# Optimization experiments

Measured on AMD Instinct MI355X. Metric: run time of the kernel, lower is better.

## Reference

```python
import jax, jax.numpy as jnp
import numpy as np

B, N, CS, CZ, CH, H, PQ, PV = 1, 768, 384, 128, 16, 12, 4, 8
INF, EPS, LN_EPS = 1e5, 1e-8, 1e-5


def setup_inputs() -> dict:
    key = jax.random.key(0)
    ks = jax.random.split(key, 16)
    def nrm(k, shape, scale=0.02):
        return jax.random.normal(k, shape, dtype=jnp.float32) * scale
    return {
        "s": jax.random.normal(ks[0], (B, N, CS), jnp.float32),
        "z": jax.random.normal(ks[1], (B, N, N, CZ), jnp.float32),
        "r_rot": jax.random.normal(ks[2], (B, N, 5, 3, 3), jnp.float32),
        "r_trans": jax.random.normal(ks[3], (B, N, 5, 3), jnp.float32),
        "mask": jnp.ones((B, N, 5), jnp.float32),
        "wq": nrm(ks[4], (H * CH, CS)), "bq": jnp.zeros((H * CH,), jnp.float32),
        "wkv": nrm(ks[5], (2 * H * CH, CS)), "bkv": jnp.zeros((2 * H * CH,), jnp.float32),
        "wqp": nrm(ks[6], (H * PQ * 3, CS)), "bqp": jnp.zeros((H * PQ * 3,), jnp.float32),
        "wkvp": nrm(ks[7], (H * (PQ + PV) * 3, CS)), "bkvp": jnp.zeros((H * (PQ + PV) * 3,), jnp.float32),
        "wb": nrm(ks[8], (H, CZ)), "bb": jnp.zeros((H,), jnp.float32),
        "head_w": nrm(ks[9], (H,), 0.5),
        "wout": nrm(ks[10], (CS, H * (CZ + CH + PV * 4))), "bout": jnp.zeros((CS,), jnp.float32),
        "wexp": nrm(ks[11], (5 * CS, CS)), "bexp": jnp.zeros((5 * CS,), jnp.float32),
        "ln_g": jnp.ones((CS,), jnp.float32), "ln_b": jnp.zeros((CS,), jnp.float32),
        "ww": nrm(ks[12], (1, CS)), "bw": jnp.zeros((1,), jnp.float32),
    }


def _mix(x, fg_mask, weight, ndims):
    # x: [B,N,5,...]; weighted blend of backbone frame (index 0) and mean of
    # masked functional-group frames (indices 1:5).
    bb_f = x[:, :, :1]
    m = fg_mask.reshape(fg_mask.shape + (1,) * ndims)
    fg = (x[:, :, 1:] * m).sum(axis=2, keepdims=True)
    denom = fg_mask.sum(-1, keepdims=True).reshape(fg_mask.shape[:2] + (1,) * (ndims + 1))
    fg = fg / (denom + 1e-8)
    w = weight.reshape(weight.shape[:2] + (1,) * (ndims + 1))
    return (w * bb_f + (1.0 - w) * fg)[:, :, 0]


def _ipa(s, z, r_rot, r_trans, mask, wq, bq, wkv, bkv, wqp, bqp, wkvp, bkvp,
         wb, bb, head_w, wout, bout, wexp, bexp, ln_g, ln_b, ww, bw):
    fg_mask = mask[..., 1:]            # [B,N,4]
    ulr = mask[..., 0]                 # [B,N]
    # softmax over a size-1 axis (as in original code -> all ones)
    weight = jax.nn.softmax(s @ ww.T + bw, axis=-1)   # [B,N,1]

    se = (s @ wexp.T + bexp).reshape(B, N, 5, CS)
    mu = se.mean(-1, keepdims=True)
    var = ((se - mu) ** 2).mean(-1, keepdims=True)
    se = (se - mu) * jax.lax.rsqrt(var + LN_EPS) * ln_g + ln_b

    q = _mix((se @ wq.T + bq).reshape(B, N, 5, H, CH), fg_mask, weight, 2)      # [B,N,H,CH]
    kv = _mix((se @ wkv.T + bkv).reshape(B, N, 5, H, 2 * CH), fg_mask, weight, 2)
    k, v = kv[..., :CH], kv[..., CH:]

    def pts_of(w_, b_, npts):
        lin = se @ w_.T + b_                                   # [B,N,5,3*H*npts]
        pts = jnp.moveaxis(lin.reshape(B, N, 5, 3, H * npts), -2, -1)  # [B,N,5,H*npts,3]
        pts = jnp.einsum('bnfij,bnfpj->bnfpi', r_rot, pts) + r_trans[:, :, :, None, :]
        return _mix(pts.reshape(B, N, 5, H, npts, 3), fg_mask, weight, 3)

    q_pts = pts_of(wqp, bqp, PQ)                               # [B,N,H,PQ,3]
    kv_pts = pts_of(wkvp, bkvp, PQ + PV)
    k_pts, v_pts = kv_pts[..., :PQ, :], kv_pts[..., PQ:, :]

    bias = z @ wb.T + bb                                       # [B,N,N,H]
    a = jnp.einsum('bihc,bjhc->bhij', q, k) * (1.0 / (3 * CH)) ** 0.5
    a = a + (1.0 / 3.0) ** 0.5 * jnp.transpose(bias, (0, 3, 1, 2))

    d2 = jnp.sum((q_pts[:, :, None] - k_pts[:, None]) ** 2, axis=-1)  # [B,N,N,H,PQ]
    hw = jax.nn.softplus(head_w) * (1.0 / (3 * (PQ * 9.0 / 2))) ** 0.5
    pt_att = -0.5 * jnp.sum(d2 * hw[:, None], axis=-1)         # [B,N,N,H]
    a = a + jnp.transpose(pt_att, (0, 3, 1, 2))
    sq_mask = INF * (ulr[:, :, None] * ulr[:, None, :] - 1.0)
    a = jax.nn.softmax(a + sq_mask[:, None], axis=-1)          # [B,H,N,N]

    o = jnp.einsum('bhij,bjhc->bihc', a, v).reshape(B, N, H * CH)
    o_pt = jnp.einsum('bhij,bjhpx->bihpx', a, v_pts)           # [B,N,H,PV,3]
    rot0, t0 = r_rot[:, :, 0], r_trans[:, :, 0]                # backbone frame
    # invert_apply: R^T (x - t)
    o_pt = jnp.einsum('bnik,bnhpi->bnhpk', rot0, o_pt - t0[:, :, None, None, :])
    o_pt_norm = jnp.sqrt(jnp.sum(o_pt ** 2, -1) + EPS).reshape(B, N, H * PV)
    o_pt = o_pt.reshape(B, N, H * PV, 3)
    o_pair = jnp.einsum('bhij,bijc->bihc', a, z).reshape(B, N, H * CZ)
    cat = jnp.concatenate([o, o_pt[..., 0], o_pt[..., 1], o_pt[..., 2], o_pt_norm, o_pair], -1)
    return cat @ wout.T + bout                                 # [B,N,CS]


def reference(s, z, r_rot, r_trans, mask, wq, bq, wkv, bkv, wqp, bqp, wkvp, bkvp,
              wb, bb, head_w, wout, bout, wexp, bexp, ln_g, ln_b, ww, bw):
    return _ipa(s, z, r_rot, r_trans, mask, wq, bq, wkv, bkv, wqp, bqp, wkvp, bkvp,
                wb, bb, head_w, wout, bout, wexp, bexp, ln_g, ln_b, ww, bw)
```

## Files before the change

### kernel.cpp

```cpp
#include <hip/hip_runtime.h>
#include <hip/hip_bf16.h>
#include <stdint.h>


typedef float  f32x4 __attribute__((ext_vector_type(4)));
typedef short  s16x8 __attribute__((ext_vector_type(8)));

__device__ __forceinline__ float bf2f(unsigned short u) {
    union { unsigned int i; float f; } v; v.i = ((unsigned int)u) << 16; return v.f;
}
__device__ __forceinline__ unsigned short f2bf(float f) {
    union { float f; unsigned int i; } v; v.f = f;
    unsigned int r = v.i + 0x7fffu + ((v.i >> 16) & 1u);
    return (unsigned short)(r >> 16);
}
__device__ __forceinline__ unsigned packbf2(float a, float b) {
    return (unsigned)f2bf(a) | ((unsigned)f2bf(b) << 16);
}
__device__ __forceinline__ float bval(int c,
    const float* bq, const float* bkv, const float* bqp, const float* bkvp)
{
    if (c < 192)      return bq[c];
    else if (c < 576) return bkv[c - 192];
    else if (c < 720) return bqp[c - 576];
    else              return bkvp[c - 720];
}

__global__ __launch_bounds__(256) void k_prep(
    const float* __restrict__ s, const float* __restrict__ wexp,
    const float* __restrict__ wq, const float* __restrict__ wkv,
    const float* __restrict__ wqp, const float* __restrict__ wkvp,
    const float* __restrict__ wout,
    const float* __restrict__ bq, const float* __restrict__ bkv,
    const float* __restrict__ bqp, const float* __restrict__ bkvp,
    unsigned short* __restrict__ s_bf, unsigned short* __restrict__ we_bf,
    unsigned short* __restrict__ wc_bf, unsigned short* __restrict__ wo_bf,
    float* __restrict__ bcat)
{
    const int x = blockIdx.x * 256 + threadIdx.x;
    if (x >= 1696896) return;
    if (x < 294912)            s_bf[x] = f2bf(s[x]);
    else if (x < 442368)       we_bf[x - 294912] = f2bf(wexp[x - 294912]);
    else if (x < 516096)       wc_bf[x - 442368] = f2bf(wq[x - 442368]);
    else if (x < 663552)       wc_bf[73728 + (x - 516096)] = f2bf(wkv[x - 516096]);
    else if (x < 718848)       wc_bf[221184 + (x - 663552)] = f2bf(wqp[x - 663552]);
    else if (x < 884736)       wc_bf[276480 + (x - 718848)] = f2bf(wkvp[x - 718848]);
    else if (x < 1695744)      wo_bf[x - 884736] = f2bf(wout[x - 884736]);
    else {
        int j = x - 1695744;
        bcat[j] = bval(j, bq, bkv, bqp, bkvp);
    }
}

__global__ __launch_bounds__(256) void k_mm(
    const unsigned short* __restrict__ A, int lda,
    const unsigned short* __restrict__ B, int ldb,
    float* __restrict__ C, int ldc, const float* __restrict__ bias,
    int nk, size_t pstride)
{
    const int m0 = blockIdx.x * 64, n0 = blockIdx.y * 64;
    const int koff = blockIdx.z * nk * 32;
    C += (size_t)blockIdx.z * pstride;
    const int t = threadIdx.x;
    const int lane = t & 63, wave = t >> 6, quad = lane >> 4, lcol = lane & 15;
    const int mh = (wave & 1) * 32, nh = (wave >> 1) * 32;
    __shared__ unsigned short As[64 * 40];
    __shared__ unsigned short Bs[64 * 40];
    const int lr = t >> 2, ls = (t & 3) * 8;
    const unsigned short* Ap = A + (size_t)(m0 + lr) * lda + koff + ls;
    const unsigned short* Bp = B + (size_t)(n0 + lr) * ldb + koff + ls;
    f32x4 acc[2][2] = {};

    uint4 av = *(const uint4*)Ap;
    uint4 bv = *(const uint4*)Bp;
    for (int kc = 0; kc < nk; ++kc) {
        __syncthreads();
        *(uint4*)&As[lr * 40 + ls] = av;
        *(uint4*)&Bs[lr * 40 + ls] = bv;
        __syncthreads();
        if (kc + 1 < nk) {
            av = *(const uint4*)(Ap + (size_t)(kc + 1) * 32);
            bv = *(const uint4*)(Bp + (size_t)(kc + 1) * 32);
        }
        s16x8 af0 = *(const s16x8*)&As[(mh + lcol) * 40 + quad * 8];
        s16x8 af1 = *(const s16x8*)&As[(mh + 16 + lcol) * 40 + quad * 8];
        s16x8 bf0 = *(const s16x8*)&Bs[(nh + lcol) * 40 + quad * 8];
        s16x8 bf1 = *(const s16x8*)&Bs[(nh + 16 + lcol) * 40 + quad * 8];
        acc[0][0] = __builtin_amdgcn_mfma_f32_16x16x32_bf16(af0, bf0, acc[0][0], 0, 0, 0);
        acc[0][1] = __builtin_amdgcn_mfma_f32_16x16x32_bf16(af0, bf1, acc[0][1], 0, 0, 0);
        acc[1][0] = __builtin_amdgcn_mfma_f32_16x16x32_bf16(af1, bf0, acc[1][0], 0, 0, 0);
        acc[1][1] = __builtin_amdgcn_mfma_f32_16x16x32_bf16(af1, bf1, acc[1][1], 0, 0, 0);
    }
    #pragma unroll
    for (int r = 0; r < 2; ++r)
        #pragma unroll
        for (int c = 0; c < 2; ++c) {
            int gn = n0 + nh + c * 16 + lcol;
            float bv2 = bias ? bias[gn] : 0.f;
            #pragma unroll
            for (int ii = 0; ii < 4; ++ii) {
                int gm = m0 + mh + r * 16 + quad * 4 + ii;
                C[(size_t)gm * ldc + gn] = acc[r][c][ii] + bv2;
            }
        }
}

__global__ __launch_bounds__(256) void k_ln(
    const float* __restrict__ se_raw, const float* __restrict__ ln_g,
    const float* __restrict__ ln_b, unsigned short* __restrict__ se0_bf)
{
    const int n = blockIdx.x * 4 + (threadIdx.x >> 6);
    const int lane = threadIdx.x & 63;
    const float* row = se_raw + (size_t)n * 384;
    float v[6], s1 = 0.f, s2 = 0.f;
    #pragma unroll
    for (int q = 0; q < 6; ++q) {
        v[q] = row[lane + q * 64];
        s1 += v[q]; s2 += v[q] * v[q];
    }
    for (int mk = 1; mk < 64; mk <<= 1) {
        s1 += __shfl_xor(s1, mk, 64);
        s2 += __shfl_xor(s2, mk, 64);
    }
    float mu = s1 * (1.f / 384.f);
    float var = s2 * (1.f / 384.f) - mu * mu;
    float rs = rsqrtf(fmaxf(var, 0.f) + 1e-5f);
    unsigned short* orow = se0_bf + (size_t)n * 384;
    #pragma unroll
    for (int q = 0; q < 6; ++q) {
        int c = lane + q * 64;
        orow[c] = f2bf((v[q] - mu) * rs * ln_g[c] + ln_b[c]);
    }
}

__global__ __launch_bounds__(256) void k_post(
    const float* __restrict__ lin,
    const float* __restrict__ r_rot, const float* __restrict__ r_trans,
    float* __restrict__ q_out, unsigned short* __restrict__ k_out,
    float* __restrict__ v_out, float* __restrict__ qp_out,
    unsigned short* __restrict__ kp_out, float* __restrict__ vp_out,
    float* __restrict__ k2_out)
{
    const int n0 = blockIdx.x * 8;
    const int t = threadIdx.x;
    __shared__ float kprot[8 * 144];

    for (int r = 0; r < 8; ++r) {
        const int n = n0 + r;
        const float* lrow = lin + (size_t)n * 1152;
        const float* rot = r_rot + (size_t)n * 45;
        for (int u = t; u < 1152; u += 256) {
            if (u < 192) {
                q_out[(size_t)n * 192 + u] = lrow[u];
            } else if (u < 576) {
                int l2 = u - 192, h = l2 >> 5, c = l2 & 31;
                float v = lrow[u];
                if (c < 16) k_out[(size_t)n * 192 + h * 16 + c] = f2bf(v);
                else        v_out[(size_t)n * 192 + h * 16 + (c - 16)] = v;
            } else {
                int y = u - 576;
                int pt = y / 3, i = y - pt * 3;
                float t0 = r_trans[(size_t)n * 15 + i];
                float v;
                if (pt < 48) {
                    v = rot[i*3+0] * lrow[576 + pt]
                      + rot[i*3+1] * lrow[576 + 48 + pt]
                      + rot[i*3+2] * lrow[576 + 96 + pt] + t0;
                    qp_out[(size_t)n * 144 + pt * 3 + i] = v;
                } else {
                    int pp = pt - 48;
                    v = rot[i*3+0] * lrow[720 + pp]
                      + rot[i*3+1] * lrow[720 + 144 + pp]
                      + rot[i*3+2] * lrow[720 + 288 + pp] + t0;
                    int h = pp / 12, pl = pp - h * 12;
                    if (pl < 4) {
                        kp_out[(size_t)n * 144 + (h * 4 + pl) * 3 + i] = f2bf(v);
                        kprot[r * 144 + (h * 4 + pl) * 3 + i] = v;
                    } else {
                        vp_out[(size_t)n * 288 + (h * 8 + (pl - 4)) * 3 + i] = v;
                    }
                }
            }
        }
    }
    __syncthreads();
    if (t < 96) {
        int r = t / 12, h = t - r * 12;
        float ss = 0.f;
        #pragma unroll
        for (int d = 0; d < 12; ++d) {
            float v = kprot[r * 144 + h * 12 + d];
            ss += v * v;
        }
        k2_out[(size_t)(n0 + r) * 12 + h] = ss;
    }
}

__global__ __launch_bounds__(256) void k_attn(
    const float* __restrict__ z, const float* __restrict__ mask,
    const float* __restrict__ head_w, const float* __restrict__ wb,
    const float* __restrict__ bb,
    const float* __restrict__ q_ws, const float* __restrict__ qp_ws,
    const float* __restrict__ k2_ws,
    const unsigned short* __restrict__ k_bf, const float* __restrict__ v_f,
    const unsigned short* __restrict__ kp_bf, const float* __restrict__ vp_f,
    float* __restrict__ parts)
{
    const int i = blockIdx.x >> 1;
    const int half = blockIdx.x & 1;
    const int t = threadIdx.x;
    const int lane = t & 63, wv = t >> 6;
    const int quad = lane >> 4, lcol = lane & 15;

    __shared__ short zb[64 * 136];
    __shared__ float L[64 * 17];
    __shared__ float Pt[16 * 68];
    __shared__ float qs[192], qps[144];
    __shared__ float ulra[384];
    __shared__ float m_s[16], l_s[16], alph_s[16];

    const float c_qk = 0.14433756729740643f;
    const float c_b  = 0.57735026918962576f;

    if (t < 192) qs[t]  = q_ws[(size_t)i * 192 + t];
    if (t < 144) qps[t] = qp_ws[(size_t)i * 144 + t];
    if (t >= 192 && t < 208) { int u = t - 192; m_s[u] = -1e30f; l_s[u] = 0.f; alph_s[u] = 1.f; }
    for (int x = t; x < 384; x += 256) ulra[x] = mask[(size_t)(half * 384 + x) * 5];
    for (int x = t; x < 4 * 68; x += 256) Pt[12 * 68 + x] = 0.f;
    const float ulr_i = mask[(size_t)i * 5];

    s16x8 wbf[4];
    #pragma unroll
    for (int kb = 0; kb < 4; ++kb) {
        #pragma unroll
        for (int j = 0; j < 8; ++j) {
            int c = kb * 32 + quad * 8 + j;
            wbf[kb][j] = (lcol < 12) ? (short)f2bf(wb[(size_t)lcol * 128 + c]) : (short)0;
        }
    }
    __syncthreads();

    const int hh = (lcol < 12) ? lcol : 11;
    f32x4 qv[4], qpv[3];
    float q2_r = 0.f;
    #pragma unroll
    for (int m = 0; m < 4; ++m) qv[m] = *(const f32x4*)&qs[hh * 16 + m * 4];
    #pragma unroll
    for (int m = 0; m < 3; ++m) {
        qpv[m] = *(const f32x4*)&qps[hh * 12 + m * 4];
        #pragma unroll
        for (int e = 0; e < 4; ++e) q2_r += qpv[m][e] * qpv[m][e];
    }
    float xh = head_w[hh];
    const float cpt_r = -0.5f * logf(1.f + __expf(xh)) * 0.13608276348795434f;
    const float cbb_r = c_b * bb[hh];

    f32x4 acc_op[2] = { {0.f,0.f,0.f,0.f}, {0.f,0.f,0.f,0.f} };
    f32x4 acc_s = {0.f,0.f,0.f,0.f};

    int vu = -1, vhalf = 0;
    if (t < 120) { vu = t; vhalf = 0; }
    else if (t >= 128 && t < 248) { vu = t - 128; vhalf = 1; }
    int vrole = -1; const float* vsrc = nullptr; int vstride = 0, voff = 0;
    if (vu >= 0) {
        if (vu < 48) { vrole = vu >> 2;       vsrc = v_f;  vstride = 192; voff = vu * 4; }
        else         { vrole = (vu - 48) / 6; vsrc = vp_f; vstride = 288; voff = (vu - 48) * 4; }
    }

    const float* zbase = z + (size_t)i * 98304 + (size_t)half * 49152;
    f32x4 zr[8];
    #pragma unroll
    for (int sx = 0; sx < 8; ++sx)
        zr[sx] = *(const f32x4*)(zbase + (size_t)(t + sx * 256) * 4);

    const int jlb = wv * 16 + quad * 4;
    const int zrow = wv * 16 + lcol;
    const int sigm = (zrow >> 3) & 3;

    for (int tt = 0; tt < 6; ++tt) {
        const int j0 = half * 384 + tt * 64;
        const int jloc0 = tt * 64;
        __syncthreads();

        #pragma unroll
        for (int sx = 0; sx < 8; ++sx) {
            int idx = t + sx * 256;
            int jl = idx >> 5, cq = idx & 31;
            int ch = (cq >> 1) ^ ((jl >> 3) & 3);
            uint2 pk;
            pk.x = packbf2(zr[sx][0], zr[sx][1]);
            pk.y = packbf2(zr[sx][2], zr[sx][3]);
            *(uint2*)&zb[jl * 136 + ch * 8 + (cq & 1) * 4] = pk;
        }
        __syncthreads();

        if (tt < 5) {
            const float* znext = zbase + (size_t)(tt + 1) * 8192;
            #pragma unroll
            for (int sx = 0; sx < 8; ++sx)
                zr[sx] = *(const f32x4*)(znext + (size_t)(t + sx * 256) * 4);
        }
        uint4 ka[4], kb4[4]; uint2 p0[4], p1[4], p2[4]; float K2r[4];
        #pragma unroll
        for (int r = 0; r < 4; ++r) {
            int jr = j0 + jlb + r;
            const unsigned short* kr = k_bf + (size_t)jr * 192 + hh * 16;
            ka[r]  = *(const uint4*)kr;
            kb4[r] = *(const uint4*)(kr + 8);
            const unsigned short* pr = kp_bf + (size_t)jr * 144 + hh * 12;
            p0[r] = *(const uint2*)pr;
            p1[r] = *(const uint2*)(pr + 4);
            p2[r] = *(const uint2*)(pr + 8);
            K2r[r] = k2_ws[(size_t)jr * 12 + hh];
        }

        f32x4 d = {0.f, 0.f, 0.f, 0.f};
        #pragma unroll
        for (int kb = 0; kb < 4; ++kb) {
            s16x8 a = *(const s16x8*)&zb[zrow * 136 + ((kb * 4 + quad) ^ sigm) * 8];
            d = __builtin_amdgcn_mfma_f32_16x16x32_bf16(a, wbf[kb], d, 0, 0, 0);
        }

        if (lcol < 12) {
            #pragma unroll
            for (int r = 0; r < 4; ++r) {
                int jl = jlb + r;
                const unsigned* kwa = (const unsigned*)&ka[r];
                const unsigned* kwb = (const unsigned*)&kb4[r];
                float qk = 0.f;
                #pragma unroll
                for (int m = 0; m < 4; ++m) {
                    qk += qv[m >> 1][(m & 1) * 2 + 0] * bf2f((unsigned short)(kwa[m] & 0xffffu));
                    qk += qv[m >> 1][(m & 1) * 2 + 1] * bf2f((unsigned short)(kwa[m] >> 16));
                }
                #pragma unroll
                for (int m = 0; m < 4; ++m) {
                    qk += qv[2 + (m >> 1)][(m & 1) * 2 + 0] * bf2f((unsigned short)(kwb[m] & 0xffffu));
                    qk += qv[2 + (m >> 1)][(m & 1) * 2 + 1] * bf2f((unsigned short)(kwb[m] >> 16));
                }
                float dp = 0.f;
                dp += qpv[0][0] * bf2f((unsigned short)(p0[r].x & 0xffffu));
                dp += qpv[0][1] * bf2f((unsigned short)(p0[r].x >> 16));
                dp += qpv[0][2] * bf2f((unsigned short)(p0[r].y & 0xffffu));
                dp += qpv[0][3] * bf2f((unsigned short)(p0[r].y >> 16));
                dp += qpv[1][0] * bf2f((unsigned short)(p1[r].x & 0xffffu));
                dp += qpv[1][1] * bf2f((unsigned short)(p1[r].x >> 16));
                dp += qpv[1][2] * bf2f((unsigned short)(p1[r].y & 0xffffu));
                dp += qpv[1][3] * bf2f((unsigned short)(p1[r].y >> 16));
                dp += qpv[2][0] * bf2f((unsigned short)(p2[r].x & 0xffffu));
                dp += qpv[2][1] * bf2f((unsigned short)(p2[r].x >> 16));
                dp += qpv[2][2] * bf2f((unsigned short)(p2[r].y & 0xffffu));
                dp += qpv[2][3] * bf2f((unsigned short)(p2[r].y >> 16));
                float ptt = cpt_r * (q2_r + K2r[r] - 2.f * dp);
                float lg = c_qk * qk + ptt + 1e5f * (ulr_i * ulra[jloc0 + jl] - 1.f)
                         + c_b * d[r] + cbb_r;
                L[jl * 17 + lcol] = lg;
            }
        }
        __syncthreads();

        if (t < 192) {
            int h = t >> 4, u = t & 15;
            float v0 = L[(u * 4 + 0) * 17 + h];
            float v1 = L[(u * 4 + 1) * 17 + h];
            float v2 = L[(u * 4 + 2) * 17 + h];
            float v3 = L[(u * 4 + 3) * 17 + h];
            float mx = fmaxf(fmaxf(v0, v1), fmaxf(v2, v3));
            for (int mk = 1; mk < 16; mk <<= 1) mx = fmaxf(mx, __shfl_xor(mx, mk, 16));
            float mold = m_s[h];
            float mnew = fmaxf(mold, mx);
            float w0 = __expf(v0 - mnew), w1 = __expf(v1 - mnew);
            float w2 = __expf(v2 - mnew), w3 = __expf(v3 - mnew);
            Pt[h * 68 + u * 4 + 0] = w0;
            Pt[h * 68 + u * 4 + 1] = w1;
            Pt[h * 68 + u * 4 + 2] = w2;
            Pt[h * 68 + u * 4 + 3] = w3;
            float sm = w0 + w1 + w2 + w3;
            for (int mk = 1; mk < 16; mk <<= 1) sm += __shfl_xor(sm, mk, 16);
            if (u == 0) {
                float al = __expf(mold - mnew);
                m_s[h] = mnew; alph_s[h] = al;
                l_s[h] = l_s[h] * al + sm;
            }
        }
        __syncthreads();

        {
            float al[4];
            #pragma unroll
            for (int r = 0; r < 4; ++r) al[r] = alph_s[quad * 4 + r];
            #pragma unroll
            for (int nt = 0; nt < 2; ++nt)
                #pragma unroll
                for (int r = 0; r < 4; ++r) acc_op[nt][r] *= al[r];
            #pragma unroll
            for (int kb = 0; kb < 2; ++kb) {
                f32x4 pa = *(const f32x4*)&Pt[lcol * 68 + kb * 32 + quad * 8];
                f32x4 pb = *(const f32x4*)&Pt[lcol * 68 + kb * 32 + quad * 8 + 4];
                union { s16x8 v; unsigned u[4]; } af;
                af.u[0] = packbf2(pa[0], pa[1]);
                af.u[1] = packbf2(pa[2], pa[3]);
                af.u[2] = packbf2(pb[0], pb[1]);
                af.u[3] = packbf2(pb[2], pb[3]);
                #pragma unroll
                for (int nt = 0; nt < 2; ++nt) {
                    int c = wv * 32 + nt * 16 + lcol;
                    int csw = ((c >> 3) ^ quad) * 8 + (c & 7);
                    s16x8 bfg;
                    #pragma unroll
                    for (int j = 0; j < 8; ++j)
                        bfg[j] = zb[(kb * 32 + quad * 8 + j) * 136 + csw];
                    acc_op[nt] = __builtin_amdgcn_mfma_f32_16x16x32_bf16(af.v, bfg, acc_op[nt], 0, 0, 0);
                }
            }
        }
        if (vu >= 0) {
            float alpha = alph_s[vrole];
            f32x4 a = acc_s;
            a[0] *= alpha; a[1] *= alpha; a[2] *= alpha; a[3] *= alpha;
            const float* prow = &Pt[vrole * 68 + vhalf * 32];
            const float* src = vsrc + (size_t)(j0 + vhalf * 32) * vstride + voff;
            #pragma unroll 4
            for (int jj = 0; jj < 32; jj += 4) {
                f32x4 p = *(const f32x4*)(prow + jj);
                #pragma unroll
                for (int m = 0; m < 4; ++m) {
                    f32x4 w = *(const f32x4*)(src + (size_t)(jj + m) * vstride);
                    float pm = p[m];
                    a[0] += pm * w[0];
                    a[1] += pm * w[1];
                    a[2] += pm * w[2];
                    a[3] += pm * w[3];
                }
            }
            acc_s = a;
        }
    }

    __syncthreads();
    float* pr = parts + (size_t)(i * 2 + half) * 2048;
    if (t < 12) { pr[2016 + t] = m_s[t]; pr[2028 + t] = l_s[t]; }
    float* vbuf = L;
    if (vu >= 0) {
        #pragma unroll
        for (int m = 0; m < 4; ++m) vbuf[(vu * 2 + vhalf) * 4 + m] = acc_s[m];
    }
    __syncthreads();
    if (t < 120) {
        float f[4];
        #pragma unroll
        for (int m = 0; m < 4; ++m)
            f[m] = vbuf[(t * 2) * 4 + m] + vbuf[(t * 2 + 1) * 4 + m];
        if (t < 48) {
            #pragma unroll
            for (int m = 0; m < 4; ++m) pr[t * 4 + m] = f[m];
        } else {
            int e0 = (t - 48) * 4;
            pr[192 + e0 + 0] = f[0]; pr[192 + e0 + 1] = f[1];
            pr[192 + e0 + 2] = f[2]; pr[192 + e0 + 3] = f[3];
        }
    }
    {
        #pragma unroll
        for (int nt = 0; nt < 2; ++nt)
            #pragma unroll
            for (int r = 0; r < 4; ++r) {
                int h = quad * 4 + r;
                if (h < 12)
                    pr[480 + h * 128 + wv * 32 + nt * 16 + lcol] = acc_op[nt][r];
            }
    }
}

__global__ __launch_bounds__(256) void k_merge(
    const float* __restrict__ parts,
    const float* __restrict__ r_rot, const float* __restrict__ r_trans,
    unsigned short* __restrict__ cat)
{
    const int i = blockIdx.x;
    const int t = threadIdx.x;
    const float* p1 = parts + (size_t)(i * 2 + 0) * 2048;
    const float* p2 = parts + (size_t)(i * 2 + 1) * 2048;
    __shared__ float w1s[12], w2s[12], lis[12];
    if (t < 12) {
        float m1 = p1[2016 + t], l1 = p1[2028 + t];
        float m2 = p2[2016 + t], l2 = p2[2028 + t];
        float m = fmaxf(m1, m2);
        float w1 = __expf(m1 - m), w2 = __expf(m2 - m);
        w1s[t] = w1; w2s[t] = w2;
        lis[t] = 1.f / (w1 * l1 + w2 * l2);
    }
    __syncthreads();
    unsigned short* crow = cat + (size_t)i * 2112;
    if (t < 192) {
        int h = t >> 4;
        crow[t] = f2bf((w1s[h] * p1[t] + w2s[h] * p2[t]) * lis[h]);
    }
    #pragma unroll
    for (int k = 0; k < 6; ++k) {
        int c = t + k * 256;
        int h = c >> 7;
        crow[576 + c] = f2bf((w1s[h] * p1[480 + c] + w2s[h] * p2[480 + c]) * lis[h]);
    }
    if (t < 96) {
        int hp = t, h = hp >> 3;
        const float* rot = r_rot + (size_t)i * 45;
        float o0 = (w1s[h] * p1[192 + hp * 3 + 0] + w2s[h] * p2[192 + hp * 3 + 0]) * lis[h];
        float o1 = (w1s[h] * p1[192 + hp * 3 + 1] + w2s[h] * p2[192 + hp * 3 + 1]) * lis[h];
        float o2 = (w1s[h] * p1[192 + hp * 3 + 2] + w2s[h] * p2[192 + hp * 3 + 2]) * lis[h];
        float d0 = o0 - r_trans[(size_t)i * 15 + 0];
        float d1 = o1 - r_trans[(size_t)i * 15 + 1];
        float d2 = o2 - r_trans[(size_t)i * 15 + 2];
        float f0 = rot[0] * d0 + rot[3] * d1 + rot[6] * d2;
        float f1 = rot[1] * d0 + rot[4] * d1 + rot[7] * d2;
        float f2 = rot[2] * d0 + rot[5] * d1 + rot[8] * d2;
        crow[192 + hp] = f2bf(f0);
        crow[288 + hp] = f2bf(f1);
        crow[384 + hp] = f2bf(f2);
        crow[480 + hp] = f2bf(sqrtf(f0 * f0 + f1 * f1 + f2 * f2 + 1e-8f));
    }
}

__global__ __launch_bounds__(256) void k_out_red(
    const float* __restrict__ parts, const float* __restrict__ bout,
    float* __restrict__ out)
{
    const int x = blockIdx.x * 256 + threadIdx.x;
    float s = bout[x % 384];
    #pragma unroll
    for (int p = 0; p < 6; ++p) s += parts[(size_t)p * 294912 + x];
    out[x] = s;
}

extern "C" void kernel_launch(void* const* d_in, const int* in_sizes, int n_in,
                              void* d_out, int out_size, void* d_ws, size_t ws_size,
                              hipStream_t stream)
{
    const float* s       = (const float*)d_in[0];
    const float* z       = (const float*)d_in[1];
    const float* r_rot   = (const float*)d_in[2];
    const float* r_trans = (const float*)d_in[3];
    const float* mask    = (const float*)d_in[4];
    const float* wq      = (const float*)d_in[5];
    const float* bq      = (const float*)d_in[6];
    const float* wkv     = (const float*)d_in[7];
    const float* bkv     = (const float*)d_in[8];
    const float* wqp     = (const float*)d_in[9];
    const float* bqp     = (const float*)d_in[10];
    const float* wkvp    = (const float*)d_in[11];
    const float* bkvp    = (const float*)d_in[12];
    const float* wb      = (const float*)d_in[13];
    const float* bb      = (const float*)d_in[14];
    const float* head_w  = (const float*)d_in[15];
    const float* wout    = (const float*)d_in[16];
    const float* bout    = (const float*)d_in[17];
    const float* wexp    = (const float*)d_in[18];
    const float* bexp    = (const float*)d_in[19];
    const float* ln_g    = (const float*)d_in[20];
    const float* ln_b    = (const float*)d_in[21];

    float* wsf = (float*)d_ws;
    float* se_raw = wsf;
    float* lin    = wsf + 294912;
    float* qf     = wsf + 1179648;
    float* qpf    = wsf + 1327104;
    float* k2w    = wsf + 1437696;
    float* bcat   = wsf + 1446912;
    float* gparts = wsf + 1448064;
    float* vf     = wsf + 3217536;
    float* vpf    = wsf + 3364992;
    unsigned short* ub = (unsigned short*)(wsf + 3586176);
    unsigned short* s_bf   = ub;
    unsigned short* we_bf  = ub + 294912;
    unsigned short* wc_bf  = ub + 442368;
    unsigned short* wo_bf  = ub + 884736;
    unsigned short* se0_bf = ub + 1695744;
    unsigned short* kbf    = ub + 1990656;
    unsigned short* kpbf   = ub + 2138112;
    unsigned short* cat_bf = ub + 2248704;
    float* pa_ws  = wsf + 5521536;
    float* out = (float*)d_out;

    k_prep<<<6629, 256, 0, stream>>>(s, wexp, wq, wkv, wqp, wkvp, wout,
                                     bq, bkv, bqp, bkvp,
                                     s_bf, we_bf, wc_bf, wo_bf, bcat);
    k_mm<<<dim3(12, 6, 1), 256, 0, stream>>>(s_bf, 384, we_bf, 384,
                                             se_raw, 384, bexp, 12, 0);
    k_ln<<<192, 256, 0, stream>>>(se_raw, ln_g, ln_b, se0_bf);
    k_mm<<<dim3(12, 18, 1), 256, 0, stream>>>(se0_bf, 384, wc_bf, 384,
                                              lin, 1152, bcat, 12, 0);
    k_post<<<96, 256, 0, stream>>>(lin, r_rot, r_trans,
                                   qf, kbf, vf, qpf, kpbf, vpf, k2w);
    k_attn<<<1536, 256, 0, stream>>>(z, mask, head_w, wb, bb,
                                     qf, qpf, k2w, kbf, vf, kpbf, vpf, pa_ws);
    k_merge<<<768, 256, 0, stream>>>(pa_ws, r_rot, r_trans, cat_bf);
    k_mm<<<dim3(12, 6, 6), 256, 0, stream>>>(cat_bf, 2112, wo_bf, 2112,
                                             gparts, 384, nullptr, 11, 294912);
    k_out_red<<<1152, 256, 0, stream>>>(gparts, bout, out);
}
```

Before: 559.6 us.

## Compute P·V and P·Vpts with bf16 MFMA using a transposed V layout

The post-projection kernel now writes V and V-points as a single bf16, transposed (feature-major, node-contiguous) buffer instead of fp32 row-major arrays. The attention kernel replaces its scalar FMA loop over probabilities and V with 16x16x32 bf16 MFMAs that reuse the probability fragment already built for the pair-bias product, keeping 8 extra accumulators per lane. The aim is to remove the scalar V accumulation, its extra barriers and the cross-half reduction through shared memory. In exchange it adds register pressure, loads B fragments directly from global memory, wastes most MFMA output by keeping only diagonal head blocks, and lowers V precision to bf16.

Result: slower. 676.7 us (+20.9%).

```diff
diff --git a/kernel.cpp b/kernel.cpp
--- a/kernel.cpp
+++ b/kernel.cpp
@@ -137,9 +137,8 @@
     const float* __restrict__ lin,
     const float* __restrict__ r_rot, const float* __restrict__ r_trans,
     float* __restrict__ q_out, unsigned short* __restrict__ k_out,
-    float* __restrict__ v_out, float* __restrict__ qp_out,
-    unsigned short* __restrict__ kp_out, float* __restrict__ vp_out,
-    float* __restrict__ k2_out)
+    float* __restrict__ qp_out, unsigned short* __restrict__ kp_out,
+    unsigned short* __restrict__ vcatT, float* __restrict__ k2_out)
 {
     const int n0 = blockIdx.x * 8;
     const int t = threadIdx.x;
@@ -156,7 +155,7 @@
                 int l2 = u - 192, h = l2 >> 5, c = l2 & 31;
                 float v = lrow[u];
                 if (c < 16) k_out[(size_t)n * 192 + h * 16 + c] = f2bf(v);
-                else        v_out[(size_t)n * 192 + h * 16 + (c - 16)] = v;
+                else        vcatT[(size_t)(h * 16 + (c - 16)) * 768 + n] = f2bf(v);
             } else {
                 int y = u - 576;
                 int pt = y / 3, i = y - pt * 3;
@@ -177,7 +176,7 @@
                         kp_out[(size_t)n * 144 + (h * 4 + pl) * 3 + i] = f2bf(v);
                         kprot[r * 144 + (h * 4 + pl) * 3 + i] = v;
                     } else {
-                        vp_out[(size_t)n * 288 + (h * 8 + (pl - 4)) * 3 + i] = v;
+                        vcatT[(size_t)(192 + (h * 8 + (pl - 4)) * 3 + i) * 768 + n] = f2bf(v);
                     }
                 }
             }
@@ -202,8 +201,8 @@
     const float* __restrict__ bb,
     const float* __restrict__ q_ws, const float* __restrict__ qp_ws,
     const float* __restrict__ k2_ws,
-    const unsigned short* __restrict__ k_bf, const float* __restrict__ v_f,
-    const unsigned short* __restrict__ kp_bf, const float* __restrict__ vp_f,
+    const unsigned short* __restrict__ k_bf, const unsigned short* __restrict__ kp_bf,
+    const unsigned short* __restrict__ vcatT,
     float* __restrict__ parts)
 {
     const int i = blockIdx.x >> 1;
@@ -256,16 +255,7 @@
     const float cbb_r = c_b * bb[hh];
 
     f32x4 acc_op[2] = { {0.f,0.f,0.f,0.f}, {0.f,0.f,0.f,0.f} };
-    f32x4 acc_s = {0.f,0.f,0.f,0.f};
-
-    int vu = -1, vhalf = 0;
-    if (t < 120) { vu = t; vhalf = 0; }
-    else if (t >= 128 && t < 248) { vu = t - 128; vhalf = 1; }
-    int vrole = -1; const float* vsrc = nullptr; int vstride = 0, voff = 0;
-    if (vu >= 0) {
-        if (vu < 48) { vrole = vu >> 2;       vsrc = v_f;  vstride = 192; voff = vu * 4; }
-        else         { vrole = (vu - 48) / 6; vsrc = vp_f; vstride = 288; voff = (vu - 48) * 4; }
-    }
+    f32x4 acc_v[8] = {};
 
     const float* zbase = z + (size_t)i * 98304 + (size_t)half * 49152;
     f32x4 zr[8];
@@ -394,6 +384,11 @@
                 #pragma unroll
                 for (int r = 0; r < 4; ++r) acc_op[nt][r] *= al[r];
             #pragma unroll
+            for (int q = 0; q < 8; ++q)
+                #pragma unroll
+                for (int r = 0; r < 4; ++r) acc_v[q][r] *= al[r];
+
+            #pragma unroll
             for (int kb = 0; kb < 2; ++kb) {
                 f32x4 pa = *(const f32x4*)&Pt[lcol * 68 + kb * 32 + quad * 8];
                 f32x4 pb = *(const f32x4*)&Pt[lcol * 68 + kb * 32 + quad * 8 + 4];
@@ -412,54 +407,22 @@
                         bfg[j] = zb[(kb * 32 + quad * 8 + j) * 136 + csw];
                     acc_op[nt] = __builtin_amdgcn_mfma_f32_16x16x32_bf16(af.v, bfg, acc_op[nt], 0, 0, 0);
                 }
-            }
-        }
-        if (vu >= 0) {
-            float alpha = alph_s[vrole];
-            f32x4 a = acc_s;
-            a[0] *= alpha; a[1] *= alpha; a[2] *= alpha; a[3] *= alpha;
-            const float* prow = &Pt[vrole * 68 + vhalf * 32];
-            const float* src = vsrc + (size_t)(j0 + vhalf * 32) * vstride + voff;
-            #pragma unroll 4
-            for (int jj = 0; jj < 32; jj += 4) {
-                f32x4 p = *(const f32x4*)(prow + jj);
-                #pragma unroll
-                for (int m = 0; m < 4; ++m) {
-                    f32x4 w = *(const f32x4*)(src + (size_t)(jj + m) * vstride);
-                    float pm = p[m];
-                    a[0] += pm * w[0];
-                    a[1] += pm * w[1];
-                    a[2] += pm * w[2];
-                    a[3] += pm * w[3];
+                #pragma unroll
+                for (int q = 0; q < 8; ++q) {
+                    int nt = wv + 4 * q;
+                    if (nt < 30) {
+                        const unsigned short* src = vcatT
+                            + (size_t)(nt * 16 + lcol) * 768 + j0 + kb * 32 + quad * 8;
+                        s16x8 bfr = *(const s16x8*)src;
+                        acc_v[q] = __builtin_amdgcn_mfma_f32_16x16x32_bf16(af.v, bfr, acc_v[q], 0, 0, 0);
+                    }
                 }
             }
-            acc_s = a;
-        }
-    }
-
-    __syncthreads();
+        }
+    }
+
     float* pr = parts + (size_t)(i * 2 + half) * 2048;
     if (t < 12) { pr[2016 + t] = m_s[t]; pr[2028 + t] = l_s[t]; }
-    float* vbuf = L;
-    if (vu >= 0) {
-        #pragma unroll
-        for (int m = 0; m < 4; ++m) vbuf[(vu * 2 + vhalf) * 4 + m] = acc_s[m];
-    }
-    __syncthreads();
-    if (t < 120) {
-        float f[4];
-        #pragma unroll
-        for (int m = 0; m < 4; ++m)
-            f[m] = vbuf[(t * 2) * 4 + m] + vbuf[(t * 2 + 1) * 4 + m];
-        if (t < 48) {
-            #pragma unroll
-            for (int m = 0; m < 4; ++m) pr[t * 4 + m] = f[m];
-        } else {
-            int e0 = (t - 48) * 4;
-            pr[192 + e0 + 0] = f[0]; pr[192 + e0 + 1] = f[1];
-            pr[192 + e0 + 2] = f[2]; pr[192 + e0 + 3] = f[3];
-        }
-    }
     {
         #pragma unroll
         for (int nt = 0; nt < 2; ++nt)
@@ -469,6 +432,24 @@
                 if (h < 12)
                     pr[480 + h * 128 + wv * 32 + nt * 16 + lcol] = acc_op[nt][r];
             }
+    }
+    {
+        #pragma unroll
+        for (int q = 0; q < 8; ++q) {
+            int nt = wv + 4 * q;
+            if (nt < 30) {
+                #pragma unroll
+                for (int r = 0; r < 4; ++r) {
+                    int h = quad * 4 + r;
+                    if (nt < 12) {
+                        if (h == nt) pr[nt * 16 + lcol] = acc_v[q][r];
+                    } else {
+                        int cc = nt * 16 + lcol - 192;
+                        if (h == cc / 24) pr[192 + cc] = acc_v[q][r];
+                    }
+                }
+            }
+        }
     }
 }
 
@@ -567,9 +548,7 @@
     float* k2w    = wsf + 1437696;
     float* bcat   = wsf + 1446912;
     float* gparts = wsf + 1448064;
-    float* vf     = wsf + 3217536;
-    float* vpf    = wsf + 3364992;
-    unsigned short* ub = (unsigned short*)(wsf + 3586176);
+    unsigned short* ub = (unsigned short*)(wsf + 3217536);
     unsigned short* s_bf   = ub;
     unsigned short* we_bf  = ub + 294912;
     unsigned short* wc_bf  = ub + 442368;
@@ -577,8 +556,9 @@
     unsigned short* se0_bf = ub + 1695744;
     unsigned short* kbf    = ub + 1990656;
     unsigned short* kpbf   = ub + 2138112;
-    unsigned short* cat_bf = ub + 2248704;
-    float* pa_ws  = wsf + 5521536;
+    unsigned short* vcatT  = ub + 2248704;
+    unsigned short* cat_bf = ub + 2617344;
+    float* pa_ws  = wsf + 5337216;
     float* out = (float*)d_out;
 
     k_prep<<<6629, 256, 0, stream>>>(s, wexp, wq, wkv, wqp, wkvp, wout,
@@ -590,9 +570,9 @@
     k_mm<<<dim3(12, 18, 1), 256, 0, stream>>>(se0_bf, 384, wc_bf, 384,
                                               lin, 1152, bcat, 12, 0);
     k_post<<<96, 256, 0, stream>>>(lin, r_rot, r_trans,
-                                   qf, kbf, vf, qpf, kpbf, vpf, k2w);
+                                   qf, kbf, qpf, kpbf, vcatT, k2w);
     k_attn<<<1536, 256, 0, stream>>>(z, mask, head_w, wb, bb,
-                                     qf, qpf, k2w, kbf, vf, kpbf, vpf, pa_ws);
+                                     qf, qpf, k2w, kbf, kpbf, vcatT, pa_ws);
     k_merge<<<768, 256, 0, stream>>>(pa_ws, r_rot, r_trans, cat_bf);
     k_mm<<<dim3(12, 6, 6), 256, 0, stream>>>(cat_bf, 2112, wo_bf, 2112,
                                              gparts, 384, nullptr, 11, 294912);
```
